# Kernel tuning notes

Measured on AMD Instinct MI355X. Metric: run time of the kernel, lower is better.

The kernel has to match this reference:

```python
import jax, jax.numpy as jnp
import numpy as np

D_MODEL = 1024
N_HEADS = 16
HEAD_DIM = D_MODEL // N_HEADS


def setup_inputs() -> dict:
    key = jax.random.key(0)
    k1, k2, k3, k4, k5 = jax.random.split(key, 5)
    s = 0.02
    return {
        "x": jax.random.normal(k1, (2, 2048, D_MODEL), dtype=jnp.float32),
        "w_qkv": jax.random.normal(k2, (D_MODEL, 3 * D_MODEL), dtype=jnp.float32) * s,
        "b_qkv": jax.random.normal(k3, (3 * D_MODEL,), dtype=jnp.float32) * s,
        "w_proj": jax.random.normal(k4, (D_MODEL, D_MODEL), dtype=jnp.float32) * s,
        "b_proj": jax.random.normal(k5, (D_MODEL,), dtype=jnp.float32) * s,
    }


def reference(x, w_qkv, b_qkv, w_proj, b_proj):
    B, T, C = x.shape
    # fused qkv projection: [B,T,3C] -> [3,B,H,T,Dh]
    qkv = x @ w_qkv + b_qkv
    qkv = qkv.reshape(B, T, 3, N_HEADS, HEAD_DIM).transpose(2, 0, 3, 1, 4)
    q, k, v = qkv[0], qkv[1], qkv[2]
    scale = 1.0 / np.sqrt(HEAD_DIM).astype(np.float32)
    att = jnp.einsum("bhtd,bhsd->bhts", q, k) * scale  # [B,H,T,T]
    causal = jnp.triu(jnp.ones((T, T), dtype=bool), k=1)
    att = jnp.where(causal, -jnp.inf, att)
    att = jax.nn.softmax(att, axis=-1)
    # dropout is identity in eval / p=0
    out = jnp.einsum("bhts,bhsd->bhtd", att, v)  # [B,H,T,Dh]
    out = out.transpose(0, 2, 1, 3).reshape(B, T, C)
    return out @ w_proj + b_proj
```

## Files before the change

kernel.cpp:

```cpp
#include <hip/hip_runtime.h>
#include <hip/hip_bf16.h>
#include <stdint.h>

#define MROWS 4096
#define DMODEL 1024
#define NQKV 3072
#define TSEQ 2048

typedef __attribute__((ext_vector_type(8))) short short8;
typedef __attribute__((ext_vector_type(4))) short short4v;
typedef __attribute__((ext_vector_type(4))) float floatx4;
typedef unsigned short ushort_t;

#define TILE_ELEMS 4608
#define BH_TILE_STRIDE 147456

#define QSCALE 0.1803368801111204f

static __device__ __forceinline__ unsigned short f2bf(float f) {
    union { float f; unsigned u; } v; v.f = f;
    unsigned r = v.u + 0x7fff + ((v.u >> 16) & 1);
    return (unsigned short)(r >> 16);
}


static __device__ __forceinline__ floatx4 mfma16(short4v a, short4v b, floatx4 c) {
#if defined(__HIP_DEVICE_COMPILE__)
#if __has_builtin(__builtin_amdgcn_mfma_f32_16x16x16bf16_1k)
    return __builtin_amdgcn_mfma_f32_16x16x16bf16_1k(a, b, c, 0, 0, 0);
#else
#error "mfma 16x16x16 bf16 builtin unavailable on device"
#endif
#else
    return c;
#endif
}

static __device__ __forceinline__ unsigned pk2bf(float a, float b) {
    unsigned ua = __float_as_uint(a) + 0x8000u;
    unsigned ub = __float_as_uint(b) + 0x8000u;
#if defined(__HIP_DEVICE_COMPILE__) && __has_builtin(__builtin_amdgcn_perm)
    return __builtin_amdgcn_perm(ub, ua, 0x07060302u);
#else
    return (ua >> 16) | (ub & 0xFFFF0000u);
#endif
}

static __device__ __forceinline__ unsigned cvtpk(float a, float b) {
#if defined(__HIP_DEVICE_COMPILE__)
    unsigned r;
    asm("v_cvt_pk_bf16_f32 %0, %1, %2" : "=v"(r) : "v"(a), "v"(b));
    return r;
#else
    return pk2bf(a, b);
#endif
}

static __device__ __forceinline__ float exp2_fast(float x) {
#if defined(__HIP_DEVICE_COMPILE__) && __has_builtin(__builtin_amdgcn_exp2f)
    return __builtin_amdgcn_exp2f(x);
#else
    return exp2f(x);
#endif
}

static __device__ __forceinline__ void glds16(const void* g, void* l) {
    __builtin_amdgcn_global_load_lds(
        (const __attribute__((address_space(1))) void*)g,
        (__attribute__((address_space(3))) void*)l, 16, 0, 0);
}

__global__ void cast_f32_bf16(const float* __restrict__ in,
                              ushort_t* __restrict__ out, int n) {
    int i = (blockIdx.x * blockDim.x + threadIdx.x) * 4;
    if (i < n) {
        float4 f = *(const float4*)(in + i);
        ushort4 o;
        o.x = f2bf(f.x); o.y = f2bf(f.y); o.z = f2bf(f.z); o.w = f2bf(f.w);
        *(ushort4*)(out + i) = o;
    }
}

__global__ void transpose_cast(const float* __restrict__ in,
                               ushort_t* __restrict__ out, int R, int C) {
    __shared__ float tile[32][33];
    int c0 = blockIdx.x * 32, r0 = blockIdx.y * 32;
    int tx = threadIdx.x & 31, ty = threadIdx.x >> 5;
    for (int i = 0; i < 4; i++) {
        int r = ty + i * 8;
        tile[r][tx] = in[(size_t)(r0 + r) * C + c0 + tx];
    }
    __syncthreads();
    for (int i = 0; i < 4; i++) {
        int r = ty + i * 8;
        out[(size_t)(c0 + r) * R + r0 + tx] = f2bf(tile[tx][r]);
    }
}

__global__ void transpose_v(const ushort_t* __restrict__ in,
                            ushort_t* __restrict__ out) {
    __shared__ ushort_t T[64][72];
    int tile = blockIdx.x, bh = blockIdx.y;
    int tid = threadIdx.x;
    int row = tid >> 2, q4 = tid & 3;
    const ushort_t* ip = in + ((size_t)bh * TSEQ + tile * 64) * 64;
#pragma unroll
    for (int p = 0; p < 2; p++) {
        int c = q4 * 16 + p * 8;
        *(uint4*)(&T[row][c]) = *(const uint4*)(ip + (size_t)row * 64 + c);
    }
    __syncthreads();
    ushort_t* op = out + (size_t)bh * BH_TILE_STRIDE + (size_t)tile * TILE_ELEMS;
#pragma unroll
    for (int p = 0; p < 2; p++) {
        int cbase = q4 * 16 + p * 8;
        ushort_t tmp[8];
#pragma unroll
        for (int e = 0; e < 8; e++) {
            int cp = cbase + e;
            int Q = cp >> 4, SB = (cp >> 2) & 3, J = cp & 3;
            int s = SB * 16 + Q * 4 + J;
            tmp[e] = T[s][row];
        }
        *(uint4*)(op + (size_t)row * 72 + cbase) = *(uint4*)tmp;
    }
}

template <int EPI, int MFRAG, int PERXCD>
__global__ __launch_bounds__(256, 3)
void gemm_glds(const ushort_t* __restrict__ A,
               const ushort_t* __restrict__ Bt,
               const float* __restrict__ bias,
               void* __restrict__ out0, void* __restrict__ out1, void* __restrict__ out2,
               int M, int N, int K) {
    __shared__ ushort_t As[2][MFRAG * 32 * 32];
    __shared__ ushort_t Bs[2][128 * 32];
    int tid = threadIdx.x;
    int wave = tid >> 6, lane = tid & 63;
    int quad = lane >> 4, l16 = lane & 15;
    int id = blockIdx.x;
    int xcd = id & 7, sidx = id >> 3;
    int m_idx = xcd * PERXCD + (sidx & (PERXCD - 1));
    int n_idx = sidx / PERXCD;
    int m0 = m_idx * (MFRAG * 32), n0 = n_idx * 128;
    int wm = (wave & 1) * (MFRAG * 16), wn = (wave >> 1) * 64;

    const floatx4 zero = {0.f, 0.f, 0.f, 0.f};
    floatx4 acc[MFRAG][4];
#pragma unroll
    for (int i = 0; i < MFRAG; i++)
#pragma unroll
        for (int j = 0; j < 4; j++) acc[i][j] = zero;

    int srow = tid >> 2, sc = tid & 3;
    const ushort_t* ag = A  + (size_t)(m0 + srow) * K + sc * 8;
    const ushort_t* bg = Bt + (size_t)(n0 + srow) * K + sc * 8;
    int woff = wave * 512;

    glds16(ag, &As[0][woff]);
    if (MFRAG == 4) glds16(ag + (size_t)64 * K, &As[0][woff + 2048]);
    glds16(bg, &Bs[0][woff]);
    glds16(bg + (size_t)64 * K, &Bs[0][woff + 2048]);
    __syncthreads();

    int cur = 0;
    for (int k0 = 0; k0 < K; k0 += 32) {
        if (k0 + 32 < K) {
            int nb = cur ^ 1, kn = k0 + 32;
            glds16(ag + kn, &As[nb][woff]);
            if (MFRAG == 4) glds16(ag + (size_t)64 * K + kn, &As[nb][woff + 2048]);
            glds16(bg + kn, &Bs[nb][woff]);
            glds16(bg + (size_t)64 * K + kn, &Bs[nb][woff + 2048]);
        }
        short8 af[MFRAG], bf[4];
#pragma unroll
        for (int i = 0; i < MFRAG; i++)
            af[i] = *(const short8*)(&As[cur][(wm + i * 16 + l16) * 32 + quad * 8]);
#pragma unroll
        for (int j = 0; j < 4; j++)
            bf[j] = *(const short8*)(&Bs[cur][(wn + j * 16 + l16) * 32 + quad * 8]);
#pragma unroll
        for (int i = 0; i < MFRAG; i++)
#pragma unroll
            for (int j = 0; j < 4; j++)
                acc[i][j] = __builtin_amdgcn_mfma_f32_16x16x32_bf16(
                    af[i], bf[j], acc[i][j], 0, 0, 0);
        __syncthreads();
        cur ^= 1;
    }

    int sec = n0 >> 10;
    ushort_t* dst = (ushort_t*)(sec == 0 ? out0 : (sec == 1 ? out1 : out2));

    if (EPI == 1 && sec == 2) {
#pragma unroll
        for (int i = 0; i < MFRAG; i++) {
            int row = m0 + wm + i * 16 + quad * 4;
            int Abits = ((wm >> 4) + i) & 3;
            int b = row >> 11, t = row & 2047;
            int tile = t >> 6;
            int colp = 16 * quad + 4 * Abits;
#pragma unroll
            for (int j = 0; j < 4; j++) {
                int col = n0 + wn + j * 16 + l16;
                int within = col & 1023, h = within >> 6, d = within & 63;
                size_t bh = (size_t)(b * 16 + h);
                float bvs = bias[col];
                ushort4 o;
                o.x = f2bf(acc[i][j][0] + bvs);
                o.y = f2bf(acc[i][j][1] + bvs);
                o.z = f2bf(acc[i][j][2] + bvs);
                o.w = f2bf(acc[i][j][3] + bvs);
                *(ushort4*)(dst + bh * BH_TILE_STRIDE + (size_t)tile * TILE_ELEMS
                            + (size_t)d * 72 + colp) = o;
            }
        }
        return;
    }

#pragma unroll
    for (int i = 0; i < MFRAG; i++) {
        int row = m0 + wm + i * 16 + quad * 4;
#pragma unroll
        for (int j = 0; j < 4; j++) {
            int col = n0 + wn + j * 16 + l16;
            float bvs = bias[col];
#pragma unroll
            for (int r = 0; r < 4; r++) {
                float v = acc[i][j][r] + bvs;
                int rowr = row + r;
                if (EPI == 0) {
                    ((float*)out0)[(size_t)rowr * N + col] = v;
                } else {
                    int b = rowr >> 11, t = rowr & 2047;
                    int within = col & 1023, h = within >> 6, d = within & 63;
                    size_t bh = (size_t)(b * 16 + h);
                    if (sec == 0)
                        dst[(bh * 2048 + t) * 64 + d] = f2bf(v * QSCALE);
                    else if (sec == 1)
                        dst[bh * BH_TILE_STRIDE + (size_t)(t >> 6) * TILE_ELEMS
                            + (size_t)(t & 63) * 72 + d] = f2bf(v);
                    else
                        dst[(bh * 2048 + t) * 64 + d] = f2bf(v);
                }
            }
        }
    }
}

__global__ __launch_bounds__(256, 4)
void attn_split(const ushort_t* __restrict__ Qb,
                const ushort_t* __restrict__ Kt,
                const ushort_t* __restrict__ Vt,
                ushort_t* __restrict__ outb,
                float* __restrict__ PO_a, float* __restrict__ PO_b,
                float* __restrict__ Pl_a, float* __restrict__ Pl_b) {
    __shared__ ushort_t Ks[2][64 * 72];
    __shared__ ushort_t Vs[2][64 * 72];
    int tid = threadIdx.x;
    int wave = tid >> 6, lane = tid & 63;
    int quad = lane >> 4, l16 = lane & 15;
    int id = blockIdx.x;
    int g = id >> 3;
    int bh = (id & 7) * 4 + (g >> 5);
    int rem = g & 31;
    int p = rem >> 1, sub = rem & 1;
    int b = bh >> 4, h = bh & 15;
    const ushort_t* qh = Qb + (size_t)bh * TSEQ * 64;
    const ushort_t* kh = Kt + (size_t)bh * BH_TILE_STRIDE;
    const ushort_t* vh = Vt + (size_t)bh * BH_TILE_STRIDE;
    const floatx4 zero = {0.f, 0.f, 0.f, 0.f};
    const short4v ones = {(short)0x3F80, (short)0x3F80, (short)0x3F80, (short)0x3F80};
    int lo8 = lane * 8;

    int nseg = sub ? 1 : 2;
    for (int seg = 0; seg < nseg; seg++) {
        int qt, k0, cnt, mode;
        if (sub)           { qt = 31 - p; k0 = 16 - p; cnt = 16;     mode = 2; }
        else if (seg == 0) { qt = p;      k0 = 0;      cnt = p + 1;  mode = 0; }
        else               { qt = 31 - p; k0 = 0;      cnt = 16 - p; mode = 1; }

        int qrow = qt * 64 + wave * 16 + l16;
        short8 qf0 = *(const short8*)(qh + (size_t)qrow * 64 + quad * 8);
        short8 qf1 = *(const short8*)(qh + (size_t)qrow * 64 + 32 + quad * 8);

        floatx4 Oacc[4];
#pragma unroll
        for (int j = 0; j < 4; j++) Oacc[j] = zero;
        floatx4 lacc = zero;

        __syncthreads();
        {
            const ushort_t* kt0 = kh + (size_t)k0 * TILE_ELEMS;
            const ushort_t* vt0 = vh + (size_t)k0 * TILE_ELEMS;
#pragma unroll
            for (int c = 0; c < 3; c++) {
                int cc = wave + 4 * c;
                if (cc < 9) {
                    glds16(kt0 + cc * 512 + lo8, &Ks[0][cc * 512]);
                    glds16(vt0 + cc * 512 + lo8, &Vs[0][cc * 512]);
                }
            }
        }

        for (int step = 0; step < cnt; step++) {
            int cur = step & 1;
            __syncthreads();
            if (step + 1 < cnt) {
                const ushort_t* kt = kh + (size_t)(k0 + step + 1) * TILE_ELEMS;
                const ushort_t* vt = vh + (size_t)(k0 + step + 1) * TILE_ELEMS;
#pragma unroll
                for (int c = 0; c < 3; c++) {
                    int cc = wave + 4 * c;
                    if (cc < 9) {
                        glds16(kt + cc * 512 + lo8, &Ks[cur ^ 1][cc * 512]);
                        glds16(vt + cc * 512 + lo8, &Vs[cur ^ 1][cc * 512]);
                    }
                }
            }
            const ushort_t* ks = &Ks[cur][0];
            const ushort_t* vs = &Vs[cur][0];

            floatx4 S[4];
            __builtin_amdgcn_s_setprio(1);
#pragma unroll
            for (int sb = 0; sb < 4; sb++) {
                short8 kf0 = *(const short8*)(ks + (sb * 16 + l16) * 72 + quad * 8);
                short8 kf1 = *(const short8*)(ks + (sb * 16 + l16) * 72 + 32 + quad * 8);
                floatx4 s = zero;
                s = __builtin_amdgcn_mfma_f32_16x16x32_bf16(kf0, qf0, s, 0, 0, 0);
                s = __builtin_amdgcn_mfma_f32_16x16x32_bf16(kf1, qf1, s, 0, 0, 0);
                S[sb] = s;
            }
            __builtin_amdgcn_s_setprio(0);
            if (k0 + step == qt) {
                int ql = wave * 16 + l16;
#pragma unroll
                for (int sb = 0; sb < 4; sb++)
#pragma unroll
                    for (int r = 0; r < 4; r++)
                        if (sb * 16 + quad * 4 + r > ql) S[sb][r] = -1e30f;
            }
#pragma unroll
            for (int sb = 0; sb < 4; sb++)
#pragma unroll
                for (int r = 0; r < 4; r++)
                    S[sb][r] = exp2_fast(S[sb][r]);

            short4v pf[4];
#pragma unroll
            for (int sb = 0; sb < 4; sb++) {
                union { unsigned u[2]; short4v v; } pk;
                pk.u[0] = cvtpk(S[sb][0], S[sb][1]);
                pk.u[1] = cvtpk(S[sb][2], S[sb][3]);
                pf[sb] = pk.v;
            }
            __builtin_amdgcn_s_setprio(1);
            lacc = mfma16(ones, pf[0], lacc);
            lacc = mfma16(ones, pf[1], lacc);
            lacc = mfma16(ones, pf[2], lacc);
            lacc = mfma16(ones, pf[3], lacc);
#pragma unroll
            for (int jd = 0; jd < 4; jd++) {
                const ushort_t* vrow = vs + (jd * 16 + l16) * 72 + quad * 16;
                short8 vA = *(const short8*)(vrow);
                short8 vB = *(const short8*)(vrow + 8);
                short4v v0 = __builtin_shufflevector(vA, vA, 0, 1, 2, 3);
                short4v v1 = __builtin_shufflevector(vA, vA, 4, 5, 6, 7);
                short4v v2 = __builtin_shufflevector(vB, vB, 0, 1, 2, 3);
                short4v v3 = __builtin_shufflevector(vB, vB, 4, 5, 6, 7);
                Oacc[jd] = mfma16(v0, pf[0], Oacc[jd]);
                Oacc[jd] = mfma16(v1, pf[1], Oacc[jd]);
                Oacc[jd] = mfma16(v2, pf[2], Oacc[jd]);
                Oacc[jd] = mfma16(v3, pf[3], Oacc[jd]);
            }
            __builtin_amdgcn_s_setprio(0);
        }

        if (mode == 0) {
            float rl = 1.0f / lacc[0];
            int row = b * TSEQ + qt * 64 + wave * 16 + l16;
#pragma unroll
            for (int jd = 0; jd < 4; jd++) {
                int col = h * 64 + jd * 16 + quad * 4;
                ushort4 o;
                o.x = f2bf(Oacc[jd][0] * rl);
                o.y = f2bf(Oacc[jd][1] * rl);
                o.z = f2bf(Oacc[jd][2] * rl);
                o.w = f2bf(Oacc[jd][3] * rl);
                *(ushort4*)(outb + (size_t)row * DMODEL + col) = o;
            }
        } else {
            float* PO = (mode == 1) ? PO_a : PO_b;
            float* Pl = (mode == 1) ? Pl_a : Pl_b;
            int prow = (qt - 16) * 64 + wave * 16 + l16;
            size_t rbase = ((size_t)bh * 1024 + prow) * 64;
#pragma unroll
            for (int jd = 0; jd < 4; jd++)
                *(floatx4*)(PO + rbase + jd * 16 + quad * 4) = Oacc[jd];
            if (quad == 0) Pl[(size_t)bh * 1024 + prow] = lacc[0];
        }
    }
}

__global__ void attn_combine(const float* __restrict__ PO_a,
                             const float* __restrict__ PO_b,
                             const float* __restrict__ Pl_a,
                             const float* __restrict__ Pl_b,
                             ushort_t* __restrict__ outb) {
    int i = blockIdx.x * 256 + threadIdx.x;
    int row = i >> 4;
    int c4 = (i & 15) * 4;
    float rl = 1.0f / (Pl_a[row] + Pl_b[row]);
    floatx4 a = *(const floatx4*)(PO_a + (size_t)row * 64 + c4);
    floatx4 c = *(const floatx4*)(PO_b + (size_t)row * 64 + c4);
    int bh = row >> 10, prow = row & 1023;
    int b = bh >> 4, h = bh & 15;
    int orow = b * TSEQ + 1024 + prow;
    ushort4 o;
    o.x = f2bf((a[0] + c[0]) * rl);
    o.y = f2bf((a[1] + c[1]) * rl);
    o.z = f2bf((a[2] + c[2]) * rl);
    o.w = f2bf((a[3] + c[3]) * rl);
    *(ushort4*)(outb + (size_t)orow * DMODEL + h * 64 + c4) = o;
}

__global__ __launch_bounds__(256, 1)
void attn_paired(const ushort_t* __restrict__ Qb,
                 const ushort_t* __restrict__ Kt,
                 const ushort_t* __restrict__ Vt,
                 ushort_t* __restrict__ outb) {
    __shared__ ushort_t Ks[2][64 * 72];
    __shared__ ushort_t Vs[2][64 * 72];
    int tid = threadIdx.x;
    int wave = tid >> 6, lane = tid & 63;
    int quad = lane >> 4, l16 = lane & 15;
    int pair = blockIdx.x;
    int bh = blockIdx.y;
    int b = bh >> 4, h = bh & 15;
    const ushort_t* qh = Qb + (size_t)bh * TSEQ * 64;
    const ushort_t* kh = Kt + (size_t)bh * BH_TILE_STRIDE;
    const ushort_t* vh = Vt + (size_t)bh * BH_TILE_STRIDE;
    const floatx4 zero = {0.f, 0.f, 0.f, 0.f};
    int lo8 = lane * 8;

    for (int half = 0; half < 2; half++) {
        int qt = half ? (31 - pair) : pair;
        int q0 = qt * 64;
        int nsteps = qt + 1;

        int qrow = q0 + wave * 16 + l16;
        short8 qf0 = *(const short8*)(qh + (size_t)qrow * 64 + quad * 8);
        short8 qf1 = *(const short8*)(qh + (size_t)qrow * 64 + 32 + quad * 8);

        floatx4 Oacc[4];
#pragma unroll
        for (int j = 0; j < 4; j++) Oacc[j] = zero;
        float lsum = 0.f;

#pragma unroll
        for (int c = 0; c < 3; c++) {
            int cc = wave + 4 * c;
            if (cc < 9) {
                glds16(kh + cc * 512 + lo8, &Ks[0][cc * 512]);
                glds16(vh + cc * 512 + lo8, &Vs[0][cc * 512]);
            }
        }

        for (int step = 0; step < nsteps; step++) {
            int cur = step & 1;
            __syncthreads();
            if (step + 1 < nsteps) {
                const ushort_t* kt = kh + (size_t)(step + 1) * TILE_ELEMS;
                const ushort_t* vt = vh + (size_t)(step + 1) * TILE_ELEMS;
#pragma unroll
                for (int c = 0; c < 3; c++) {
                    int cc = wave + 4 * c;
                    if (cc < 9) {
                        glds16(kt + cc * 512 + lo8, &Ks[cur ^ 1][cc * 512]);
                        glds16(vt + cc * 512 + lo8, &Vs[cur ^ 1][cc * 512]);
                    }
                }
            }
            const ushort_t* ks = &Ks[cur][0];
            const ushort_t* vs = &Vs[cur][0];

            floatx4 S[4];
#pragma unroll
            for (int sb = 0; sb < 4; sb++) {
                short8 kf0 = *(const short8*)(ks + (sb * 16 + l16) * 72 + quad * 8);
                short8 kf1 = *(const short8*)(ks + (sb * 16 + l16) * 72 + 32 + quad * 8);
                floatx4 s = zero;
                s = __builtin_amdgcn_mfma_f32_16x16x32_bf16(kf0, qf0, s, 0, 0, 0);
                s = __builtin_amdgcn_mfma_f32_16x16x32_bf16(kf1, qf1, s, 0, 0, 0);
                S[sb] = s;
            }
            if (step == nsteps - 1) {
                int ql = wave * 16 + l16;
#pragma unroll
                for (int sb = 0; sb < 4; sb++)
#pragma unroll
                    for (int r = 0; r < 4; r++)
                        if (sb * 16 + quad * 4 + r > ql) S[sb][r] = -1e30f;
            }
            float sum = 0.f;
#pragma unroll
            for (int sb = 0; sb < 4; sb++)
#pragma unroll
                for (int r = 0; r < 4; r++) {
                    float p = exp2_fast(S[sb][r]);
                    S[sb][r] = p;
                    sum += p;
                }
            lsum += sum;

            short4v pf[4];
#pragma unroll
            for (int sb = 0; sb < 4; sb++) {
                union { unsigned u[2]; short4v v; } pk;
                pk.u[0] = pk2bf(S[sb][0], S[sb][1]);
                pk.u[1] = pk2bf(S[sb][2], S[sb][3]);
                pf[sb] = pk.v;
            }
#pragma unroll
            for (int jd = 0; jd < 4; jd++) {
                const ushort_t* vrow = vs + (jd * 16 + l16) * 72 + quad * 16;
                short8 vA = *(const short8*)(vrow);
                short8 vB = *(const short8*)(vrow + 8);
                short4v v0 = __builtin_shufflevector(vA, vA, 0, 1, 2, 3);
                short4v v1 = __builtin_shufflevector(vA, vA, 4, 5, 6, 7);
                short4v v2 = __builtin_shufflevector(vB, vB, 0, 1, 2, 3);
                short4v v3 = __builtin_shufflevector(vB, vB, 4, 5, 6, 7);
                Oacc[jd] = mfma16(v0, pf[0], Oacc[jd]);
                Oacc[jd] = mfma16(v1, pf[1], Oacc[jd]);
                Oacc[jd] = mfma16(v2, pf[2], Oacc[jd]);
                Oacc[jd] = mfma16(v3, pf[3], Oacc[jd]);
            }
        }
        {
            float l = lsum;
            l += __shfl_xor(l, 16);
            l += __shfl_xor(l, 32);
            float rl = 1.0f / l;
            int row = b * TSEQ + q0 + wave * 16 + l16;
#pragma unroll
            for (int jd = 0; jd < 4; jd++) {
                int col = h * 64 + jd * 16 + quad * 4;
                ushort4 o;
                o.x = f2bf(Oacc[jd][0] * rl);
                o.y = f2bf(Oacc[jd][1] * rl);
                o.z = f2bf(Oacc[jd][2] * rl);
                o.w = f2bf(Oacc[jd][3] * rl);
                *(ushort4*)(outb + (size_t)row * DMODEL + col) = o;
            }
        }
        __syncthreads();
    }
}

extern "C" void kernel_launch(void* const* d_in, const int* in_sizes, int n_in,
                              void* d_out, int out_size, void* d_ws, size_t ws_size,
                              hipStream_t stream) {
    const float* x      = (const float*)d_in[0];
    const float* w_qkv  = (const float*)d_in[1];
    const float* b_qkv  = (const float*)d_in[2];
    const float* w_proj = (const float*)d_in[3];
    const float* b_proj = (const float*)d_in[4];
    float* out = (float*)d_out;
    char* ws = (char*)d_ws;

    ushort_t* xb     = (ushort_t*)(ws);
    ushort_t* wqkvT  = (ushort_t*)(ws + 8388608);
    ushort_t* wprojT = (ushort_t*)(ws + 10485760);
    ushort_t* Qb     = (ushort_t*)(ws + 14680064);
    ushort_t* Kt     = (ushort_t*)(ws + 23068672);
    ushort_t* attnb  = (ushort_t*)(ws + 32505856);
    ushort_t* Vt     = (ushort_t*)(ws + 40894464);
    float* PO_a = (float*)(ws + 50331648);
    float* PO_b = (float*)(ws + 58720256);
    float* Pl_a = (float*)(ws + 67108864);
    float* Pl_b = (float*)(ws + 67239936);
    const size_t ws_need = 67371008;

    cast_f32_bf16<<<4096, 256, 0, stream>>>(x, xb, MROWS * DMODEL);
    transpose_cast<<<dim3(NQKV / 32, DMODEL / 32), 256, 0, stream>>>(w_qkv, wqkvT, DMODEL, NQKV);

    if (ws_size >= ws_need) {
        gemm_glds<1, 4, 4><<<768, 256, 0, stream>>>(
            xb, wqkvT, b_qkv, Qb, Kt, Vt, MROWS, NQKV, DMODEL);
        transpose_cast<<<dim3(DMODEL / 32, DMODEL / 32), 256, 0, stream>>>(w_proj, wprojT, DMODEL, DMODEL);
        attn_split<<<dim3(1024), 256, 0, stream>>>(Qb, Kt, Vt, attnb,
                                                   PO_a, PO_b, Pl_a, Pl_b);
        attn_combine<<<dim3(2048), 256, 0, stream>>>(PO_a, PO_b, Pl_a, Pl_b, attnb);
    } else {
        ushort_t* Vb    = (ushort_t*)(ws + 32505856);
        ushort_t* VtOld = (ushort_t*)(ws);
        gemm_glds<2, 4, 4><<<768, 256, 0, stream>>>(
            xb, wqkvT, b_qkv, Qb, Kt, Vb, MROWS, NQKV, DMODEL);
        transpose_v<<<dim3(32, 32), 256, 0, stream>>>(Vb, VtOld);
        transpose_cast<<<dim3(DMODEL / 32, DMODEL / 32), 256, 0, stream>>>(w_proj, wprojT, DMODEL, DMODEL);
        attn_paired<<<dim3(16, 32), 256, 0, stream>>>(Qb, Kt, VtOld, Vb);
    }

    gemm_glds<0, 2, 8><<<512, 256, 0, stream>>>(
        attnb, wprojT, b_proj, out, nullptr, nullptr, MROWS, DMODEL, DMODEL);
}
```

Before: 180.7 us.

## Process two 16-row query slabs per wave in attn_split with 128-thread blocks

Halves the attention block to two waves, each handling 32 query rows as two 16-row MFMA slabs, so every K and V fragment loaded from LDS is reused across two query slabs. This cuts LDS reads per MFMA and the per-step synchronisation overhead per unit of work. The cost is higher register pressure (double accumulators and probabilities), fewer waves per block to issue the global-to-LDS tile copies, and a changed occupancy target in launch bounds.

```diff
diff --git a/kernel.cpp b/kernel.cpp
--- a/kernel.cpp
+++ b/kernel.cpp
@@ -248,7 +248,7 @@
     }
 }
 
-__global__ __launch_bounds__(256, 4)
+__global__ __launch_bounds__(128, 2)
 void attn_split(const ushort_t* __restrict__ Qb,
                 const ushort_t* __restrict__ Kt,
                 const ushort_t* __restrict__ Vt,
@@ -280,22 +280,29 @@
         else if (seg == 0) { qt = p;      k0 = 0;      cnt = p + 1;  mode = 0; }
         else               { qt = 31 - p; k0 = 0;      cnt = 16 - p; mode = 1; }
 
-        int qrow = qt * 64 + wave * 16 + l16;
-        short8 qf0 = *(const short8*)(qh + (size_t)qrow * 64 + quad * 8);
-        short8 qf1 = *(const short8*)(qh + (size_t)qrow * 64 + 32 + quad * 8);
-
-        floatx4 Oacc[4];
-#pragma unroll
-        for (int j = 0; j < 4; j++) Oacc[j] = zero;
-        floatx4 lacc = zero;
+        short8 qf0[2], qf1[2];
+#pragma unroll
+        for (int qs = 0; qs < 2; qs++) {
+            int qrow = qt * 64 + wave * 32 + qs * 16 + l16;
+            qf0[qs] = *(const short8*)(qh + (size_t)qrow * 64 + quad * 8);
+            qf1[qs] = *(const short8*)(qh + (size_t)qrow * 64 + 32 + quad * 8);
+        }
+
+        floatx4 Oacc[2][4];
+#pragma unroll
+        for (int qs = 0; qs < 2; qs++)
+#pragma unroll
+            for (int j = 0; j < 4; j++) Oacc[qs][j] = zero;
+        floatx4 lacc[2];
+        lacc[0] = zero; lacc[1] = zero;
 
         __syncthreads();
         {
             const ushort_t* kt0 = kh + (size_t)k0 * TILE_ELEMS;
             const ushort_t* vt0 = vh + (size_t)k0 * TILE_ELEMS;
 #pragma unroll
-            for (int c = 0; c < 3; c++) {
-                int cc = wave + 4 * c;
+            for (int c = 0; c < 5; c++) {
+                int cc = wave + 2 * c;
                 if (cc < 9) {
                     glds16(kt0 + cc * 512 + lo8, &Ks[0][cc * 512]);
                     glds16(vt0 + cc * 512 + lo8, &Vs[0][cc * 512]);
@@ -310,8 +317,8 @@
                 const ushort_t* kt = kh + (size_t)(k0 + step + 1) * TILE_ELEMS;
                 const ushort_t* vt = vh + (size_t)(k0 + step + 1) * TILE_ELEMS;
 #pragma unroll
-                for (int c = 0; c < 3; c++) {
-                    int cc = wave + 4 * c;
+                for (int c = 0; c < 5; c++) {
+                    int cc = wave + 2 * c;
                     if (cc < 9) {
                         glds16(kt + cc * 512 + lo8, &Ks[cur ^ 1][cc * 512]);
                         glds16(vt + cc * 512 + lo8, &Vs[cur ^ 1][cc * 512]);
@@ -321,45 +328,58 @@
             const ushort_t* ks = &Ks[cur][0];
             const ushort_t* vs = &Vs[cur][0];
 
-            floatx4 S[4];
+            floatx4 S[2][4];
             __builtin_amdgcn_s_setprio(1);
 #pragma unroll
             for (int sb = 0; sb < 4; sb++) {
                 short8 kf0 = *(const short8*)(ks + (sb * 16 + l16) * 72 + quad * 8);
                 short8 kf1 = *(const short8*)(ks + (sb * 16 + l16) * 72 + 32 + quad * 8);
-                floatx4 s = zero;
-                s = __builtin_amdgcn_mfma_f32_16x16x32_bf16(kf0, qf0, s, 0, 0, 0);
-                s = __builtin_amdgcn_mfma_f32_16x16x32_bf16(kf1, qf1, s, 0, 0, 0);
-                S[sb] = s;
+#pragma unroll
+                for (int qs = 0; qs < 2; qs++) {
+                    floatx4 s = zero;
+                    s = __builtin_amdgcn_mfma_f32_16x16x32_bf16(kf0, qf0[qs], s, 0, 0, 0);
+                    s = __builtin_amdgcn_mfma_f32_16x16x32_bf16(kf1, qf1[qs], s, 0, 0, 0);
+                    S[qs][sb] = s;
+                }
             }
             __builtin_amdgcn_s_setprio(0);
             if (k0 + step == qt) {
-                int ql = wave * 16 + l16;
+#pragma unroll
+                for (int qs = 0; qs < 2; qs++) {
+                    int ql = wave * 32 + qs * 16 + l16;
+#pragma unroll
+                    for (int sb = 0; sb < 4; sb++)
+#pragma unroll
+                        for (int r = 0; r < 4; r++)
+                            if (sb * 16 + quad * 4 + r > ql) S[qs][sb][r] = -1e30f;
+                }
+            }
+#pragma unroll
+            for (int qs = 0; qs < 2; qs++)
 #pragma unroll
                 for (int sb = 0; sb < 4; sb++)
 #pragma unroll
                     for (int r = 0; r < 4; r++)
-                        if (sb * 16 + quad * 4 + r > ql) S[sb][r] = -1e30f;
-            }
-#pragma unroll
-            for (int sb = 0; sb < 4; sb++)
-#pragma unroll
-                for (int r = 0; r < 4; r++)
-                    S[sb][r] = exp2_fast(S[sb][r]);
-
-            short4v pf[4];
-#pragma unroll
-            for (int sb = 0; sb < 4; sb++) {
-                union { unsigned u[2]; short4v v; } pk;
-                pk.u[0] = cvtpk(S[sb][0], S[sb][1]);
-                pk.u[1] = cvtpk(S[sb][2], S[sb][3]);
-                pf[sb] = pk.v;
-            }
+                        S[qs][sb][r] = exp2_fast(S[qs][sb][r]);
+
+            short4v pf[2][4];
+#pragma unroll
+            for (int qs = 0; qs < 2; qs++)
+#pragma unroll
+                for (int sb = 0; sb < 4; sb++) {
+                    union { unsigned u[2]; short4v v; } pk;
+                    pk.u[0] = cvtpk(S[qs][sb][0], S[qs][sb][1]);
+                    pk.u[1] = cvtpk(S[qs][sb][2], S[qs][sb][3]);
+                    pf[qs][sb] = pk.v;
+                }
             __builtin_amdgcn_s_setprio(1);
-            lacc = mfma16(ones, pf[0], lacc);
-            lacc = mfma16(ones, pf[1], lacc);
-            lacc = mfma16(ones, pf[2], lacc);
-            lacc = mfma16(ones, pf[3], lacc);
+#pragma unroll
+            for (int qs = 0; qs < 2; qs++) {
+                lacc[qs] = mfma16(ones, pf[qs][0], lacc[qs]);
+                lacc[qs] = mfma16(ones, pf[qs][1], lacc[qs]);
+                lacc[qs] = mfma16(ones, pf[qs][2], lacc[qs]);
+                lacc[qs] = mfma16(ones, pf[qs][3], lacc[qs]);
+            }
 #pragma unroll
             for (int jd = 0; jd < 4; jd++) {
                 const ushort_t* vrow = vs + (jd * 16 + l16) * 72 + quad * 16;
@@ -369,36 +389,45 @@
                 short4v v1 = __builtin_shufflevector(vA, vA, 4, 5, 6, 7);
                 short4v v2 = __builtin_shufflevector(vB, vB, 0, 1, 2, 3);
                 short4v v3 = __builtin_shufflevector(vB, vB, 4, 5, 6, 7);
-                Oacc[jd] = mfma16(v0, pf[0], Oacc[jd]);
-                Oacc[jd] = mfma16(v1, pf[1], Oacc[jd]);
-                Oacc[jd] = mfma16(v2, pf[2], Oacc[jd]);
-                Oacc[jd] = mfma16(v3, pf[3], Oacc[jd]);
+#pragma unroll
+                for (int qs = 0; qs < 2; qs++) {
+                    Oacc[qs][jd] = mfma16(v0, pf[qs][0], Oacc[qs][jd]);
+                    Oacc[qs][jd] = mfma16(v1, pf[qs][1], Oacc[qs][jd]);
+                    Oacc[qs][jd] = mfma16(v2, pf[qs][2], Oacc[qs][jd]);
+                    Oacc[qs][jd] = mfma16(v3, pf[qs][3], Oacc[qs][jd]);
+                }
             }
             __builtin_amdgcn_s_setprio(0);
         }
 
         if (mode == 0) {
-            float rl = 1.0f / lacc[0];
-            int row = b * TSEQ + qt * 64 + wave * 16 + l16;
-#pragma unroll
-            for (int jd = 0; jd < 4; jd++) {
-                int col = h * 64 + jd * 16 + quad * 4;
-                ushort4 o;
-                o.x = f2bf(Oacc[jd][0] * rl);
-                o.y = f2bf(Oacc[jd][1] * rl);
-                o.z = f2bf(Oacc[jd][2] * rl);
-                o.w = f2bf(Oacc[jd][3] * rl);
-                *(ushort4*)(outb + (size_t)row * DMODEL + col) = o;
+#pragma unroll
+            for (int qs = 0; qs < 2; qs++) {
+                float rl = 1.0f / lacc[qs][0];
+                int row = b * TSEQ + qt * 64 + wave * 32 + qs * 16 + l16;
+#pragma unroll
+                for (int jd = 0; jd < 4; jd++) {
+                    int col = h * 64 + jd * 16 + quad * 4;
+                    ushort4 o;
+                    o.x = f2bf(Oacc[qs][jd][0] * rl);
+                    o.y = f2bf(Oacc[qs][jd][1] * rl);
+                    o.z = f2bf(Oacc[qs][jd][2] * rl);
+                    o.w = f2bf(Oacc[qs][jd][3] * rl);
+                    *(ushort4*)(outb + (size_t)row * DMODEL + col) = o;
+                }
             }
         } else {
             float* PO = (mode == 1) ? PO_a : PO_b;
             float* Pl = (mode == 1) ? Pl_a : Pl_b;
-            int prow = (qt - 16) * 64 + wave * 16 + l16;
-            size_t rbase = ((size_t)bh * 1024 + prow) * 64;
-#pragma unroll
-            for (int jd = 0; jd < 4; jd++)
-                *(floatx4*)(PO + rbase + jd * 16 + quad * 4) = Oacc[jd];
-            if (quad == 0) Pl[(size_t)bh * 1024 + prow] = lacc[0];
+#pragma unroll
+            for (int qs = 0; qs < 2; qs++) {
+                int prow = (qt - 16) * 64 + wave * 32 + qs * 16 + l16;
+                size_t rbase = ((size_t)bh * 1024 + prow) * 64;
+#pragma unroll
+                for (int jd = 0; jd < 4; jd++)
+                    *(floatx4*)(PO + rbase + jd * 16 + quad * 4) = Oacc[qs][jd];
+                if (quad == 0) Pl[(size_t)bh * 1024 + prow] = lacc[qs][0];
+            }
         }
     }
 }
@@ -589,7 +618,7 @@
         gemm_glds<1, 4, 4><<<768, 256, 0, stream>>>(
             xb, wqkvT, b_qkv, Qb, Kt, Vt, MROWS, NQKV, DMODEL);
         transpose_cast<<<dim3(DMODEL / 32, DMODEL / 32), 256, 0, stream>>>(w_proj, wprojT, DMODEL, DMODEL);
-        attn_split<<<dim3(1024), 256, 0, stream>>>(Qb, Kt, Vt, attnb,
+        attn_split<<<dim3(1024), 128, 0, stream>>>(Qb, Kt, Vt, attnb,
                                                    PO_a, PO_b, Pl_a, Pl_b);
         attn_combine<<<dim3(2048), 256, 0, stream>>>(PO_a, PO_b, Pl_a, Pl_b, attnb);
     } else {
```

Result: no change. 180.7 us (+0.0%).
